# Performance work log

Hardware: AMD Instinct MI355X
Metric: run time of the kernel (lower is better)

Reference implementation:

```python
import jax, jax.numpy as jnp
import numpy as np

N_MOV, N_CREW, N_CAST = 200000, 100000, 100000
E = 600000
H, OUT = 128, 16


def _sage(x_src, x_dst, src, dst, Wl, Wr, b, n_dst):
    # PyG SAGEConv: lin_l(mean_{j in N(i)} x_src[j]) + lin_r(x_dst[i]); bias lives in lin_l
    msg = jax.ops.segment_sum(x_src[src], dst, num_segments=n_dst)
    cnt = jax.ops.segment_sum(jnp.ones(src.shape, x_src.dtype), dst, num_segments=n_dst)
    agg = msg / jnp.maximum(cnt, 1.0)[:, None]
    return agg @ Wl + b + x_dst @ Wr


def setup_inputs() -> dict:
    key = jax.random.key(0)
    kit = iter(jax.random.split(key, 64))
    def rn(shape, s=0.05):
        return jax.random.normal(next(kit), shape, jnp.float32) * s
    inp = {
        'x_movies': rn((N_MOV, 128), 1.0),
        'x_crew': rn((N_CREW, 64), 1.0),
        'x_cast': rn((N_CAST, 64), 1.0),
        'src_cm': jax.random.randint(next(kit), (E,), 0, N_CREW),
        'dst_cm': jax.random.randint(next(kit), (E,), 0, N_MOV),
        'src_am': jax.random.randint(next(kit), (E,), 0, N_CAST),
        'dst_am': jax.random.randint(next(kit), (E,), 0, N_MOV),
    }
    # (src_dim, dst_dim) per relation at layer 0; layer 1 uses H for both
    dims = {'cm': (64, 128), 'am': (64, 128), 'mc': (128, 64), 'ma': (128, 64)}
    for l in range(2):
        for rel, (ds, dd) in dims.items():
            if l > 0:
                ds, dd = H, H
            inp[f'Wl_{rel}_{l}'] = rn((ds, H))
            inp[f'Wr_{rel}_{l}'] = rn((dd, H))
            inp[f'b_{rel}_{l}'] = jnp.zeros((H,), jnp.float32)
    inp['lin_W'] = rn((H, OUT))
    inp['lin_b'] = jnp.zeros((OUT,), jnp.float32)
    return inp


def reference(x_movies, x_crew, x_cast, src_cm, dst_cm, src_am, dst_am,
              Wl_cm_0, Wr_cm_0, b_cm_0, Wl_am_0, Wr_am_0, b_am_0,
              Wl_mc_0, Wr_mc_0, b_mc_0, Wl_ma_0, Wr_ma_0, b_ma_0,
              Wl_cm_1, Wr_cm_1, b_cm_1, Wl_am_1, Wr_am_1, b_am_1,
              Wl_mc_1, Wr_mc_1, b_mc_1, Wl_ma_1, Wr_ma_1, b_ma_1,
              lin_W, lin_b):
    params = [
        {'cm': (Wl_cm_0, Wr_cm_0, b_cm_0), 'am': (Wl_am_0, Wr_am_0, b_am_0),
         'mc': (Wl_mc_0, Wr_mc_0, b_mc_0), 'ma': (Wl_ma_0, Wr_ma_0, b_ma_0)},
        {'cm': (Wl_cm_1, Wr_cm_1, b_cm_1), 'am': (Wl_am_1, Wr_am_1, b_am_1),
         'mc': (Wl_mc_1, Wr_mc_1, b_mc_1), 'ma': (Wl_ma_1, Wr_ma_1, b_ma_1)},
    ]
    xm, xc, xa = x_movies, x_crew, x_cast
    for p in params:  # dropout is identity in eval mode
        # movies receives from crew and cast; HeteroConv aggr='mean' over the 2 relations
        m = 0.5 * (_sage(xc, xm, src_cm, dst_cm, *p['cm'], N_MOV)
                   + _sage(xa, xm, src_am, dst_am, *p['am'], N_MOV))
        # reverse relations: movies -> crew / cast (flip edge direction)
        c = _sage(xm, xc, dst_cm, src_cm, *p['mc'], N_CREW)
        a = _sage(xm, xa, dst_am, src_am, *p['ma'], N_CAST)
        xm, xc, xa = jax.nn.relu(m), jax.nn.relu(c), jax.nn.relu(a)
    return xm @ lin_W + lin_b
```

## Files before the change

### kernel.cpp

```cpp
#include <hip/hip_runtime.h>

#define TPB 256
typedef unsigned int uint;
typedef unsigned short ushort;
typedef long long ll;
typedef __attribute__((ext_vector_type(8))) short bf16x8;
typedef __attribute__((ext_vector_type(8))) ushort u16x8;
typedef __attribute__((ext_vector_type(4))) float f32x4;

__device__ __forceinline__ float bf2f(ushort h) {
  return __uint_as_float(((uint)h) << 16);
}
__device__ __forceinline__ ushort f2bf(float f) {
  uint u = __float_as_uint(f);
  u += 0x7fffu + ((u >> 16) & 1u);
  return (ushort)(u >> 16);
}

__global__ __launch_bounds__(TPB) void convert_k(const float* __restrict__ x,
                                                 ushort* __restrict__ o, ll n8) {
  ll i = (ll)blockIdx.x * TPB + threadIdx.x;
  if (i >= n8) return;
  const float* p = x + i * 8;
  float4 a = *(const float4*)p;
  float4 b = *(const float4*)(p + 4);
  u16x8 v;
  v[0] = f2bf(a.x); v[1] = f2bf(a.y); v[2] = f2bf(a.z); v[3] = f2bf(a.w);
  v[4] = f2bf(b.x); v[5] = f2bf(b.y); v[6] = f2bf(b.z); v[7] = f2bf(b.w);
  *(u16x8*)&o[i * 8] = v;
}

__global__ __launch_bounds__(TPB) void rank_k(const int* __restrict__ src_cm,
                                              const int* __restrict__ dst_cm,
                                              const int* __restrict__ src_am,
                                              const int* __restrict__ dst_am, int E,
                                              int* __restrict__ cnt_m_cm,
                                              int* __restrict__ cnt_m_am,
                                              int* __restrict__ cnt_c,
                                              int* __restrict__ cnt_a,
                                              int* __restrict__ rk_m_cm,
                                              int* __restrict__ rk_c,
                                              int* __restrict__ rk_m_am,
                                              int* __restrict__ rk_a) {
  int i = blockIdx.x * blockDim.x + threadIdx.x;
  if (i < E) {
    rk_m_cm[i] = atomicAdd(&cnt_m_cm[dst_cm[i]], 1);
    rk_c[i]    = atomicAdd(&cnt_c[src_cm[i]], 1);
  } else if (i < 2 * E) {
    int e = i - E;
    rk_m_am[e] = atomicAdd(&cnt_m_am[dst_am[e]], 1);
    rk_a[e]    = atomicAdd(&cnt_a[src_am[e]], 1);
  }
}

__global__ __launch_bounds__(TPB) void rinvall_k(const int* __restrict__ cnt,
                                                 float* __restrict__ rinv,
                                                 int nm2, int total) {
  int i = blockIdx.x * blockDim.x + threadIdx.x;
  if (i < total) {
    float scale = (i < nm2) ? 0.5f : 1.0f;
    rinv[i] = scale / fmaxf((float)cnt[i], 1.0f);
  }
}

struct PJobs {
  const float* a[10];
  const float* bavg[10];
  ushort* out[10];
  const float* ba[2];
  const float* bb[2];
  float* bo[2];
};

__global__ __launch_bounds__(TPB) void prep_k(PJobs J) {
  int b = blockIdx.x;
  int t = threadIdx.x;
  if (b == 512) {
    if (t < 128) J.bo[0][t] = 0.5f * (J.ba[0][t] + J.bb[0][t]);
    else if (t < 256) J.bo[1][t - 128] = 0.5f * (J.ba[1][t - 128] + J.bb[1][t - 128]);
    return;
  }
  int job, idx, K;
  if (b < 384) { job = b >> 6; idx = ((b & 63) << 8) | t; K = 128; }
  else { int bb = b - 384; job = 6 + (bb >> 5); idx = ((bb & 31) << 8) | t; K = 64; }
  int col = idx / K, k = idx - col * K;
  float v = J.a[job][k * 128 + col];
  if (J.bavg[job]) v = 0.5f * (v + J.bavg[job][k * 128 + col]);
  J.out[job][idx] = f2bf(v);
}

__device__ __forceinline__ void rel_map(int b, int nb0, int nb1, int nb2, int nb3,
                                        int& r, int& lb) {
  if (b < nb0) { r = 0; lb = b; }
  else if (b < nb0 + nb1) { r = 1; lb = b - nb0; }
  else if (b < nb0 + nb1 + nb2) { r = 2; lb = b - nb0 - nb1; }
  else { r = 3; lb = b - nb0 - nb1 - nb2; }
}

__global__ __launch_bounds__(TPB) void blocksum_all_k(
    const int* __restrict__ c0, int n0, const int* __restrict__ c1, int n1,
    const int* __restrict__ c2, int n2, const int* __restrict__ c3, int n3,
    int* __restrict__ bsum) {
  __shared__ int lds[TPB];
  int nb0 = (n0 + TPB - 1) / TPB, nb1 = (n1 + TPB - 1) / TPB;
  int nb2 = (n2 + TPB - 1) / TPB, nb3 = (n3 + TPB - 1) / TPB;
  int r, lb;
  rel_map(blockIdx.x, nb0, nb1, nb2, nb3, r, lb);
  const int* cnt = (r == 0) ? c0 : (r == 1) ? c1 : (r == 2) ? c2 : c3;
  int n = (r == 0) ? n0 : (r == 1) ? n1 : (r == 2) ? n2 : n3;
  int t = threadIdx.x;
  int i = lb * TPB + t;
  lds[t] = (i < n) ? cnt[i] : 0;
  __syncthreads();
  for (int off = 128; off > 0; off >>= 1) {
    if (t < off) lds[t] += lds[t + off];
    __syncthreads();
  }
  if (t == 0) bsum[r * 1024 + lb] = lds[0];
}

__global__ __launch_bounds__(TPB) void scan_all_k(int* __restrict__ bsum,
                                                  int n0, int n1, int n2, int n3) {
  __shared__ int lds[TPB];
  int r = blockIdx.x;
  int n = (r == 0) ? n0 : (r == 1) ? n1 : (r == 2) ? n2 : n3;
  int nb = (n + TPB - 1) / TPB;
  int* bs = bsum + r * 1024;
  int t = threadIdx.x;
  int offset = 0;
  for (int base = 0; base < nb; base += TPB) {
    int v = (base + t < nb) ? bs[base + t] : 0;
    lds[t] = v;
    __syncthreads();
    for (int off = 1; off < TPB; off <<= 1) {
      int add = (t >= off) ? lds[t - off] : 0;
      __syncthreads();
      lds[t] += add;
      __syncthreads();
    }
    int incl = lds[t];
    if (base + t < nb) bs[base + t] = offset + incl - v;
    int tot = lds[TPB - 1];
    __syncthreads();
    offset += tot;
  }
}

__global__ __launch_bounds__(TPB) void finalize_all_k(
    const int* __restrict__ c0, int n0, int* __restrict__ rp0,
    const int* __restrict__ c1, int n1, int* __restrict__ rp1,
    const int* __restrict__ c2, int n2, int* __restrict__ rp2,
    const int* __restrict__ c3, int n3, int* __restrict__ rp3,
    const int* __restrict__ bsum) {
  __shared__ int lds[TPB];
  int nb0 = (n0 + TPB - 1) / TPB, nb1 = (n1 + TPB - 1) / TPB;
  int nb2 = (n2 + TPB - 1) / TPB, nb3 = (n3 + TPB - 1) / TPB;
  int r, lb;
  rel_map(blockIdx.x, nb0, nb1, nb2, nb3, r, lb);
  const int* cnt = (r == 0) ? c0 : (r == 1) ? c1 : (r == 2) ? c2 : c3;
  int* rowptr = (r == 0) ? rp0 : (r == 1) ? rp1 : (r == 2) ? rp2 : rp3;
  int n = (r == 0) ? n0 : (r == 1) ? n1 : (r == 2) ? n2 : n3;
  int t = threadIdx.x;
  int i = lb * TPB + t;
  int v = (i < n) ? cnt[i] : 0;
  lds[t] = v;
  __syncthreads();
  for (int off = 1; off < TPB; off <<= 1) {
    int add = (t >= off) ? lds[t - off] : 0;
    __syncthreads();
    lds[t] += add;
    __syncthreads();
  }
  int ex = lds[t] - v + bsum[r * 1024 + lb];
  if (i < n) {
    rowptr[i] = ex;
    if (i == n - 1) rowptr[n] = ex + v;
  }
}

__global__ __launch_bounds__(TPB) void fillr_k(const int* __restrict__ src_cm,
                                               const int* __restrict__ dst_cm,
                                               const int* __restrict__ src_am,
                                               const int* __restrict__ dst_am, int E,
                                               const int* __restrict__ rp_m_cm,
                                               const int* __restrict__ rp_m_am,
                                               const int* __restrict__ rp_c,
                                               const int* __restrict__ rp_a,
                                               const int* __restrict__ rk_m_cm,
                                               const int* __restrict__ rk_c,
                                               const int* __restrict__ rk_m_am,
                                               const int* __restrict__ rk_a,
                                               int* __restrict__ pm_m_cm,
                                               int* __restrict__ pm_m_am,
                                               int* __restrict__ pm_c,
                                               int* __restrict__ pm_a) {
  int i = blockIdx.x * blockDim.x + threadIdx.x;
  if (i < E) {
    int s = src_cm[i], d = dst_cm[i];
    pm_m_cm[rp_m_cm[d] + rk_m_cm[i]] = s;
    pm_c[rp_c[s] + rk_c[i]] = d;
  } else if (i < 2 * E) {
    int e = i - E;
    int s = src_am[e], d = dst_am[e];
    pm_m_am[rp_m_am[d] + rk_m_am[e]] = s;
    pm_a[rp_a[s] + rk_a[e]] = d;
  }
}

__global__ __launch_bounds__(TPB) void gatherw2_k(
    const ushort* __restrict__ xmh,
    const int* __restrict__ rp1, const int* __restrict__ pm1,
    const float* __restrict__ ri1, int N1, ushort* __restrict__ o1,
    const int* __restrict__ rp2, const int* __restrict__ pm2,
    const float* __restrict__ ri2, int N2, ushort* __restrict__ o2, int g1) {
  int b = blockIdx.x;
  const int* rowptr; const int* perm; const float* rinv; int N; ushort* out;
  int lb;
  if (b < g1) { rowptr = rp1; perm = pm1; rinv = ri1; N = N1; out = o1; lb = b; }
  else { rowptr = rp2; perm = pm2; rinv = ri2; N = N2; out = o2; lb = b - g1; }
  int nid = lb * 16 + (threadIdx.x >> 4);
  if (nid >= N) return;
  int d = (threadIdx.x & 15) << 3;
  int s0 = rowptr[nid], s1 = rowptr[nid + 1];
  float acc[8] = {0.f, 0.f, 0.f, 0.f, 0.f, 0.f, 0.f, 0.f};
  for (int j = s0; j < s1; ++j) {
    u16x8 v = *(const u16x8*)&xmh[((ll)perm[j] << 7) + d];
#pragma unroll
    for (int k = 0; k < 8; ++k) acc[k] += bf2f(v[k]);
  }
  float r = rinv[nid];
  u16x8 o;
#pragma unroll
  for (int k = 0; k < 8; ++k) o[k] = f2bf(acc[k] * r);
  *(u16x8*)&out[((ll)nid << 7) + d] = o;
}

__global__ __launch_bounds__(TPB) void gather2_k(
    const ushort* __restrict__ s1, const ushort* __restrict__ s2,
    const int* __restrict__ rp1, const int* __restrict__ pm1, const float* __restrict__ ri1,
    const int* __restrict__ rp2, const int* __restrict__ pm2, const float* __restrict__ ri2,
    int N, ushort* __restrict__ out) {
  int nid = blockIdx.x * 16 + (threadIdx.x >> 4);
  if (nid >= N) return;
  int d = (threadIdx.x & 15) << 3;
  float a1[8] = {0.f, 0.f, 0.f, 0.f, 0.f, 0.f, 0.f, 0.f};
  for (int j = rp1[nid]; j < rp1[nid + 1]; ++j) {
    u16x8 v = *(const u16x8*)&s1[((ll)pm1[j] << 7) + d];
#pragma unroll
    for (int k = 0; k < 8; ++k) a1[k] += bf2f(v[k]);
  }
  float a2[8] = {0.f, 0.f, 0.f, 0.f, 0.f, 0.f, 0.f, 0.f};
  for (int j = rp2[nid]; j < rp2[nid + 1]; ++j) {
    u16x8 v = *(const u16x8*)&s2[((ll)pm2[j] << 7) + d];
#pragma unroll
    for (int k = 0; k < 8; ++k) a2[k] += bf2f(v[k]);
  }
  float r1 = ri1[nid], r2 = ri2[nid];
  ushort* p = &out[((ll)nid << 7) + d];
  u16x8 cur = *(u16x8*)p;
  u16x8 o;
#pragma unroll
  for (int k = 0; k < 8; ++k) o[k] = f2bf(bf2f(cur[k]) + a1[k] * r1 + a2[k] * r2);
  *(u16x8*)p = o;
}

__global__ __launch_bounds__(TPB) void final_k(const ushort* __restrict__ X,
                                               const float* __restrict__ W,
                                               const float* __restrict__ b,
                                               float* __restrict__ out, int M) {
  __shared__ float lw[128 * 16];
  __shared__ float lb[16];
  int t = threadIdx.x;
  for (int i = t; i < 2048; i += TPB) lw[i] = W[i];
  if (t < 16) lb[t] = b[t];
  __syncthreads();
  ll row = (ll)blockIdx.x * TPB + t;
  if (row >= M) return;
  float acc[16];
#pragma unroll
  for (int c = 0; c < 16; ++c) acc[c] = lb[c];
  const ushort* xr = &X[row * 128];
  for (int k = 0; k < 128; k += 8) {
    u16x8 xv = *(const u16x8*)&xr[k];
#pragma unroll
    for (int j = 0; j < 8; ++j) {
      float xs = fmaxf(bf2f(xv[j]), 0.f);
#pragma unroll
      for (int c = 0; c < 16; ++c) acc[c] = fmaf(xs, lw[(k + j) * 16 + c], acc[c]);
    }
  }
#pragma unroll
  for (int c = 0; c < 16; c += 4) {
    float4 o; o.x = acc[c]; o.y = acc[c + 1]; o.z = acc[c + 2]; o.w = acc[c + 3];
    *(float4*)&out[row * 16 + c] = o;
  }
}

#define BK 64
#define XPITCH 72
#define CPITCH 132
struct CArgs {
  const void* X0; const ushort* WT0; int K0; int xb0;
  const void* X1; const ushort* WT1; int K1; int xb1;
  int nseg; const float* bias; void* out; int M; int nblk;
};

template <bool XRELU>
__global__ __launch_bounds__(TPB) void mfma3_k(CArgs a0, CArgs a1, CArgs a2) {
  const int bx = blockIdx.x;
  const CArgs& a = (bx < a0.nblk) ? a0 : (bx < a0.nblk + a1.nblk) ? a1 : a2;
  const int blk = (bx < a0.nblk) ? bx
                  : (bx < a0.nblk + a1.nblk) ? bx - a0.nblk
                                             : bx - a0.nblk - a1.nblk;

  __shared__ ushort sbuf[2 * 128 * XPITCH];
  ushort* Xs = sbuf;
  ushort* Ws = sbuf + 128 * XPITCH;
  const int t = threadIdx.x;
  const int lane = t & 63;
  const int wid = t >> 6;
  const int wm = (wid >> 1) << 6;
  const int wn = (wid & 1) << 6;
  const ll rbase = (ll)blk * 128;
  const int M = a.M;

  f32x4 acc[4][4];
#pragma unroll
  for (int mi = 0; mi < 4; ++mi)
#pragma unroll
    for (int ni = 0; ni < 4; ++ni) acc[mi][ni] = (f32x4){0.f, 0.f, 0.f, 0.f};

  for (int s = 0; s < a.nseg; ++s) {
    const void* Xv = s ? a.X1 : a.X0;
    const ushort* WT = s ? a.WT1 : a.WT0;
    const int K = s ? a.K1 : a.K0;
    const int xb = s ? a.xb1 : a.xb0;
    for (int k0 = 0; k0 < K; k0 += BK) {
      __syncthreads();
#pragma unroll
      for (int i = 0; i < 4; ++i) {
        int idx8 = t + i * TPB;
        int row = idx8 >> 3;
        int kb = (idx8 & 7) << 3;
        u16x8 xv;
        ll grow = rbase + row;
        if (grow < M) {
          if (xb) {
            xv = *(const u16x8*)((const ushort*)Xv + grow * K + k0 + kb);
            if (XRELU) {
#pragma unroll
              for (int j = 0; j < 8; ++j) xv[j] = (xv[j] & 0x8000u) ? (ushort)0 : xv[j];
            }
          } else {
            const float* xp = (const float*)Xv + grow * K + k0 + kb;
            float4 va = *(const float4*)xp;
            float4 vb = *(const float4*)(xp + 4);
            if (XRELU) {
              va.x = fmaxf(va.x, 0.f); va.y = fmaxf(va.y, 0.f);
              va.z = fmaxf(va.z, 0.f); va.w = fmaxf(va.w, 0.f);
              vb.x = fmaxf(vb.x, 0.f); vb.y = fmaxf(vb.y, 0.f);
              vb.z = fmaxf(vb.z, 0.f); vb.w = fmaxf(vb.w, 0.f);
            }
            xv[0] = f2bf(va.x); xv[1] = f2bf(va.y); xv[2] = f2bf(va.z); xv[3] = f2bf(va.w);
            xv[4] = f2bf(vb.x); xv[5] = f2bf(vb.y); xv[6] = f2bf(vb.z); xv[7] = f2bf(vb.w);
          }
        } else {
#pragma unroll
          for (int j = 0; j < 8; ++j) xv[j] = 0;
        }
        *(u16x8*)&Xs[row * XPITCH + kb] = xv;
        *(u16x8*)&Ws[row * XPITCH + kb] = *(const u16x8*)(WT + (ll)row * K + k0 + kb);
      }
      __syncthreads();
#pragma unroll
      for (int kk = 0; kk < BK; kk += 32) {
        const int krow = kk + ((lane >> 4) << 3);
        bf16x8 af[4], bfr[4];
#pragma unroll
        for (int mi = 0; mi < 4; ++mi)
          af[mi] = *(const bf16x8*)&Xs[(wm + mi * 16 + (lane & 15)) * XPITCH + krow];
#pragma unroll
        for (int ni = 0; ni < 4; ++ni)
          bfr[ni] = *(const bf16x8*)&Ws[(wn + ni * 16 + (lane & 15)) * XPITCH + krow];
#pragma unroll
        for (int mi = 0; mi < 4; ++mi)
#pragma unroll
          for (int ni = 0; ni < 4; ++ni)
            acc[mi][ni] = __builtin_amdgcn_mfma_f32_16x16x32_bf16(af[mi], bfr[ni],
                                                                  acc[mi][ni], 0, 0, 0);
      }
    }
  }

  __syncthreads();

  {
    const int colb = wn + (lane & 15);
    const int rsub = (lane >> 4) << 2;
#pragma unroll
    for (int ni = 0; ni < 4; ++ni) {
      int col = colb + ni * 16;
      float bv = a.bias ? a.bias[col] : 0.f;
#pragma unroll
      for (int mi = 0; mi < 4; ++mi) {
        int row0 = wm + mi * 16 + rsub;
#pragma unroll
        for (int j = 0; j < 4; ++j)
          sbuf[(row0 + j) * CPITCH + col] = f2bf(acc[mi][ni][j] + bv);
      }
    }
  }
  __syncthreads();
  {
    int lrow = t >> 1;
    int half = t & 1;
    ll grow = rbase + lrow;
    if (grow < M) {
      const ushort* src = &sbuf[lrow * CPITCH + half * 64];
      ushort* dst = (ushort*)a.out + grow * 128 + half * 64;
#pragma unroll
      for (int k = 0; k < 8; ++k)
        *(u16x8*)(dst + k * 8) = *(const u16x8*)(src + k * 8);
    }
  }
}

extern "C" void kernel_launch(void* const* d_in, const int* in_sizes, int n_in,
                              void* d_out, int out_size, void* d_ws, size_t ws_size,
                              hipStream_t stream) {
  const float* xm = (const float*)d_in[0];
  const float* xc = (const float*)d_in[1];
  const float* xa = (const float*)d_in[2];
  const int* src_cm = (const int*)d_in[3];
  const int* dst_cm = (const int*)d_in[4];
  const int* src_am = (const int*)d_in[5];
  const int* dst_am = (const int*)d_in[6];
  const float* Wl_cm_0 = (const float*)d_in[7];
  const float* Wr_cm_0 = (const float*)d_in[8];
  const float* b_cm_0  = (const float*)d_in[9];
  const float* Wl_am_0 = (const float*)d_in[10];
  const float* Wr_am_0 = (const float*)d_in[11];
  const float* b_am_0  = (const float*)d_in[12];
  const float* Wl_mc_0 = (const float*)d_in[13];
  const float* Wr_mc_0 = (const float*)d_in[14];
  const float* b_mc_0  = (const float*)d_in[15];
  const float* Wl_ma_0 = (const float*)d_in[16];
  const float* Wr_ma_0 = (const float*)d_in[17];
  const float* b_ma_0  = (const float*)d_in[18];
  const float* Wl_cm_1 = (const float*)d_in[19];
  const float* Wr_cm_1 = (const float*)d_in[20];
  const float* b_cm_1  = (const float*)d_in[21];
  const float* Wl_am_1 = (const float*)d_in[22];
  const float* Wr_am_1 = (const float*)d_in[23];
  const float* b_am_1  = (const float*)d_in[24];
  const float* lin_W   = (const float*)d_in[31];
  const float* lin_b   = (const float*)d_in[32];

  const int NM = in_sizes[0] / 128;
  const int NC = in_sizes[1] / 64;
  const int NA = in_sizes[2] / 64;
  const int E  = in_sizes[3];
  const int SMAX = (NC > NA) ? NC : NA;

  float* base = (float*)d_ws;
  size_t o = 0;
  ushort* A = (ushort*)(base + o); o += (size_t)NM * 64;
  ushort* xmh = (ushort*)(base + o); o += (size_t)NM * 64;
  float* S = base + o; o += (size_t)SMAX * 128;
  ushort* B = (ushort*)(base + o); o += (size_t)NC * 64;
  ushort* C = (ushort*)(base + o); o += (size_t)NA * 64;
  int* cnt_m_cm = (int*)(base + o); o += NM;
  int* cnt_m_am = (int*)(base + o); o += NM;
  int* cnt_c    = (int*)(base + o); o += NC;
  int* cnt_a    = (int*)(base + o); o += NA;
  float* rinv_m_cm = base + o; o += NM;
  float* rinv_m_am = base + o; o += NM;
  float* rinv_c    = base + o; o += NC;
  float* rinv_a    = base + o; o += NA;
  int* rp_m_cm = (int*)(base + o); o += NM + 1;
  int* rp_m_am = (int*)(base + o); o += NM + 1;
  int* rp_c    = (int*)(base + o); o += NC + 1;
  int* rp_a    = (int*)(base + o); o += NA + 1;
  int* pm_m_cm = (int*)(base + o); o += E;
  int* pm_m_am = (int*)(base + o); o += E;
  int* pm_c    = (int*)(base + o); o += E;
  int* pm_a    = (int*)(base + o); o += E;
  int* bsum    = (int*)(base + o); o += 4096;
  float* b0c  = base + o; o += 128;
  float* b1c  = base + o; o += 128;
  ushort* WT_r0   = (ushort*)(base + o); o += 8192;
  ushort* WT_r1   = (ushort*)(base + o); o += 8192;
  ushort* WT_mc0l = (ushort*)(base + o); o += 8192;
  ushort* WT_ma0l = (ushort*)(base + o); o += 8192;
  ushort* WT_cm1  = (ushort*)(base + o); o += 8192;
  ushort* WT_am1  = (ushort*)(base + o); o += 8192;
  ushort* WT_mc0r = (ushort*)(base + o); o += 4096;
  ushort* WT_ma0r = (ushort*)(base + o); o += 4096;
  ushort* WT_cm0  = (ushort*)(base + o); o += 4096;
  ushort* WT_am0  = (ushort*)(base + o); o += 4096;

  if (ws_size < o * sizeof(float)) return;

  int* rk_m_cm = (int*)S;
  int* rk_c    = rk_m_cm + E;
  int* rk_m_am = rk_m_cm + 2 * E;
  int* rk_a    = rk_m_cm + 3 * E;
  ushort* S1h = (ushort*)S;
  ushort* S2h = S1h + (size_t)SMAX * 128;

  float* outf = (float*)d_out;
  const int g2E = (2 * E + TPB - 1) / TPB;
  const int nbm = (NM + TPB - 1) / TPB;
  const int nbc = (NC + TPB - 1) / TPB;
  const int nba = (NA + TPB - 1) / TPB;
  const int nbtot = 2 * nbm + nbc + nba;
  const int nodes_total = 2 * NM + NC + NA;

  {
    ll n8 = (ll)NM * 16;
    convert_k<<<(int)((n8 + TPB - 1) / TPB), TPB, 0, stream>>>(xm, xmh, n8);
  }

  hipMemsetAsync(cnt_m_cm, 0, sizeof(int) * (size_t)nodes_total, stream);
  rank_k<<<g2E, TPB, 0, stream>>>(src_cm, dst_cm, src_am, dst_am, E,
                                  cnt_m_cm, cnt_m_am, cnt_c, cnt_a,
                                  rk_m_cm, rk_c, rk_m_am, rk_a);
  rinvall_k<<<(nodes_total + TPB - 1) / TPB, TPB, 0, stream>>>(cnt_m_cm, rinv_m_cm,
                                                               2 * NM, nodes_total);

  PJobs J;
  J.a[0] = Wr_cm_0; J.bavg[0] = Wr_am_0; J.out[0] = WT_r0;
  J.a[1] = Wr_cm_1; J.bavg[1] = Wr_am_1; J.out[1] = WT_r1;
  J.a[2] = Wl_mc_0; J.bavg[2] = nullptr; J.out[2] = WT_mc0l;
  J.a[3] = Wl_ma_0; J.bavg[3] = nullptr; J.out[3] = WT_ma0l;
  J.a[4] = Wl_cm_1; J.bavg[4] = nullptr; J.out[4] = WT_cm1;
  J.a[5] = Wl_am_1; J.bavg[5] = nullptr; J.out[5] = WT_am1;
  J.a[6] = Wr_mc_0; J.bavg[6] = nullptr; J.out[6] = WT_mc0r;
  J.a[7] = Wr_ma_0; J.bavg[7] = nullptr; J.out[7] = WT_ma0r;
  J.a[8] = Wl_cm_0; J.bavg[8] = nullptr; J.out[8] = WT_cm0;
  J.a[9] = Wl_am_0; J.bavg[9] = nullptr; J.out[9] = WT_am0;
  J.ba[0] = b_cm_0; J.bb[0] = b_am_0; J.bo[0] = b0c;
  J.ba[1] = b_cm_1; J.bb[1] = b_am_1; J.bo[1] = b1c;
  prep_k<<<513, TPB, 0, stream>>>(J);

  blocksum_all_k<<<nbtot, TPB, 0, stream>>>(cnt_m_cm, NM, cnt_m_am, NM,
                                            cnt_c, NC, cnt_a, NA, bsum);
  scan_all_k<<<4, TPB, 0, stream>>>(bsum, NM, NM, NC, NA);
  finalize_all_k<<<nbtot, TPB, 0, stream>>>(cnt_m_cm, NM, rp_m_cm, cnt_m_am, NM, rp_m_am,
                                            cnt_c, NC, rp_c, cnt_a, NA, rp_a, bsum);
  fillr_k<<<g2E, TPB, 0, stream>>>(src_cm, dst_cm, src_am, dst_am, E,
                                   rp_m_cm, rp_m_am, rp_c, rp_a,
                                   rk_m_cm, rk_c, rk_m_am, rk_a,
                                   pm_m_cm, pm_m_am, pm_c, pm_a);

  const int gM = (NM + 127) / 128;
  const int gC = (NC + 127) / 128;
  const int gA = (NA + 127) / 128;
  const int gnM = (NM + 15) / 16;
  const int gwc = (NC + 15) / 16;
  const int gwa = (NA + 15) / 16;
  CArgs Z = {};

  gatherw2_k<<<gwc + gwa, TPB, 0, stream>>>(xmh, rp_c, pm_c, rinv_c, NC, S1h,
                                            rp_a, pm_a, rinv_a, NA, S2h, gwc);
  {
    CArgs ac = {S1h, WT_mc0l, 128, 1, xc, WT_mc0r, 64, 0, 2, b_mc_0, B, NC, gC};
    CArgs aa = {S2h, WT_ma0l, 128, 1, xa, WT_ma0r, 64, 0, 2, b_ma_0, C, NA, gA};
    CArgs am = {xmh, WT_r0, 128, 1, nullptr, nullptr, 0, 0, 1, b0c, A, NM, gM};
    mfma3_k<false><<<gC + gA + gM, TPB, 0, stream>>>(ac, aa, am);
  }
  {
    CArgs ac = {xc, WT_cm0, 64, 0, nullptr, nullptr, 0, 0, 1, nullptr, S1h, NC, gC};
    CArgs aa = {xa, WT_am0, 64, 0, nullptr, nullptr, 0, 0, 1, nullptr, S2h, NA, gA};
    mfma3_k<false><<<gC + gA, TPB, 0, stream>>>(ac, aa, Z);
  }
  gather2_k<<<gnM, TPB, 0, stream>>>(S1h, S2h, rp_m_cm, pm_m_cm, rinv_m_cm,
                                     rp_m_am, pm_m_am, rinv_m_am, NM, A);

  {
    CArgs am = {A, WT_r1, 128, 1, nullptr, nullptr, 0, 0, 1, b1c, A, NM, gM};
    CArgs ac = {B, WT_cm1, 128, 1, nullptr, nullptr, 0, 0, 1, nullptr, S1h, NC, gC};
    CArgs aa = {C, WT_am1, 128, 1, nullptr, nullptr, 0, 0, 1, nullptr, S2h, NA, gA};
    mfma3_k<true><<<gM + gC + gA, TPB, 0, stream>>>(am, ac, aa);
  }
  gather2_k<<<gnM, TPB, 0, stream>>>(S1h, S2h, rp_m_cm, pm_m_cm, rinv_m_cm,
                                     rp_m_am, pm_m_am, rinv_m_am, NM, A);

  final_k<<<(NM + TPB - 1) / TPB, TPB, 0, stream>>>(A, lin_W, lin_b, outf, NM);
}
```

Before: 585.6 us.

## Merge prep kernels, fuse layer-0 GEMM launches, and dual-accumulate gathers

Combines the bf16 conversion, degree-ranking atomics and weight-prep blocks into one launch, and folds the reciprocal-count computation into the block-sum kernel, which removes several small launches. The two layer-0 GEMM launches become one five-job launch by writing the crew/cast transforms to new scratch buffers (S3h/S4h), so they no longer overwrite S1h/S2h. The gather kernels unroll by two with separate accumulators to raise memory-level parallelism. The extra scratch buffers add workspace, and heterogeneous blocks in one launch may compete for resources.

```diff
diff --git a/kernel.cpp b/kernel.cpp
--- a/kernel.cpp
+++ b/kernel.cpp
@@ -15,52 +15,6 @@
   uint u = __float_as_uint(f);
   u += 0x7fffu + ((u >> 16) & 1u);
   return (ushort)(u >> 16);
-}
-
-__global__ __launch_bounds__(TPB) void convert_k(const float* __restrict__ x,
-                                                 ushort* __restrict__ o, ll n8) {
-  ll i = (ll)blockIdx.x * TPB + threadIdx.x;
-  if (i >= n8) return;
-  const float* p = x + i * 8;
-  float4 a = *(const float4*)p;
-  float4 b = *(const float4*)(p + 4);
-  u16x8 v;
-  v[0] = f2bf(a.x); v[1] = f2bf(a.y); v[2] = f2bf(a.z); v[3] = f2bf(a.w);
-  v[4] = f2bf(b.x); v[5] = f2bf(b.y); v[6] = f2bf(b.z); v[7] = f2bf(b.w);
-  *(u16x8*)&o[i * 8] = v;
-}
-
-__global__ __launch_bounds__(TPB) void rank_k(const int* __restrict__ src_cm,
-                                              const int* __restrict__ dst_cm,
-                                              const int* __restrict__ src_am,
-                                              const int* __restrict__ dst_am, int E,
-                                              int* __restrict__ cnt_m_cm,
-                                              int* __restrict__ cnt_m_am,
-                                              int* __restrict__ cnt_c,
-                                              int* __restrict__ cnt_a,
-                                              int* __restrict__ rk_m_cm,
-                                              int* __restrict__ rk_c,
-                                              int* __restrict__ rk_m_am,
-                                              int* __restrict__ rk_a) {
-  int i = blockIdx.x * blockDim.x + threadIdx.x;
-  if (i < E) {
-    rk_m_cm[i] = atomicAdd(&cnt_m_cm[dst_cm[i]], 1);
-    rk_c[i]    = atomicAdd(&cnt_c[src_cm[i]], 1);
-  } else if (i < 2 * E) {
-    int e = i - E;
-    rk_m_am[e] = atomicAdd(&cnt_m_am[dst_am[e]], 1);
-    rk_a[e]    = atomicAdd(&cnt_a[src_am[e]], 1);
-  }
-}
-
-__global__ __launch_bounds__(TPB) void rinvall_k(const int* __restrict__ cnt,
-                                                 float* __restrict__ rinv,
-                                                 int nm2, int total) {
-  int i = blockIdx.x * blockDim.x + threadIdx.x;
-  if (i < total) {
-    float scale = (i < nm2) ? 0.5f : 1.0f;
-    rinv[i] = scale / fmaxf((float)cnt[i], 1.0f);
-  }
 }
 
 struct PJobs {
@@ -72,9 +26,43 @@
   float* bo[2];
 };
 
-__global__ __launch_bounds__(TPB) void prep_k(PJobs J) {
+__global__ __launch_bounds__(TPB) void mega1_k(
+    const float* __restrict__ xm, ushort* __restrict__ xmh, ll n8, int gConv,
+    const int* __restrict__ src_cm, const int* __restrict__ dst_cm,
+    const int* __restrict__ src_am, const int* __restrict__ dst_am, int E, int g2E,
+    int* __restrict__ cnt_m_cm, int* __restrict__ cnt_m_am,
+    int* __restrict__ cnt_c, int* __restrict__ cnt_a,
+    int* __restrict__ rk_m_cm, int* __restrict__ rk_c,
+    int* __restrict__ rk_m_am, int* __restrict__ rk_a,
+    PJobs J) {
   int b = blockIdx.x;
   int t = threadIdx.x;
+  if (b < gConv) {
+    ll i = (ll)b * TPB + t;
+    if (i >= n8) return;
+    const float* p = xm + i * 8;
+    float4 a = *(const float4*)p;
+    float4 bb = *(const float4*)(p + 4);
+    u16x8 v;
+    v[0] = f2bf(a.x); v[1] = f2bf(a.y); v[2] = f2bf(a.z); v[3] = f2bf(a.w);
+    v[4] = f2bf(bb.x); v[5] = f2bf(bb.y); v[6] = f2bf(bb.z); v[7] = f2bf(bb.w);
+    *(u16x8*)&xmh[i * 8] = v;
+    return;
+  }
+  b -= gConv;
+  if (b < g2E) {
+    int i = b * TPB + t;
+    if (i < E) {
+      rk_m_cm[i] = atomicAdd(&cnt_m_cm[dst_cm[i]], 1);
+      rk_c[i]    = atomicAdd(&cnt_c[src_cm[i]], 1);
+    } else if (i < 2 * E) {
+      int e = i - E;
+      rk_m_am[e] = atomicAdd(&cnt_m_am[dst_am[e]], 1);
+      rk_a[e]    = atomicAdd(&cnt_a[src_am[e]], 1);
+    }
+    return;
+  }
+  b -= g2E;
   if (b == 512) {
     if (t < 128) J.bo[0][t] = 0.5f * (J.ba[0][t] + J.bb[0][t]);
     else if (t < 256) J.bo[1][t - 128] = 0.5f * (J.ba[1][t - 128] + J.bb[1][t - 128]);
@@ -82,7 +70,7 @@
   }
   int job, idx, K;
   if (b < 384) { job = b >> 6; idx = ((b & 63) << 8) | t; K = 128; }
-  else { int bb = b - 384; job = 6 + (bb >> 5); idx = ((bb & 31) << 8) | t; K = 64; }
+  else { int bb2 = b - 384; job = 6 + (bb2 >> 5); idx = ((bb2 & 31) << 8) | t; K = 64; }
   int col = idx / K, k = idx - col * K;
   float v = J.a[job][k * 128 + col];
   if (J.bavg[job]) v = 0.5f * (v + J.bavg[job][k * 128 + col]);
@@ -97,18 +85,27 @@
   else { r = 3; lb = b - nb0 - nb1 - nb2; }
 }
 
-__global__ __launch_bounds__(TPB) void blocksum_all_k(
+__global__ __launch_bounds__(TPB) void bsum_rinv_k(
     const int* __restrict__ c0, int n0, const int* __restrict__ c1, int n1,
     const int* __restrict__ c2, int n2, const int* __restrict__ c3, int n3,
-    int* __restrict__ bsum) {
+    int* __restrict__ bsum, float* __restrict__ rinv, int nm2, int total, int nbtot) {
   __shared__ int lds[TPB];
+  int b = blockIdx.x;
+  int t = threadIdx.x;
+  if (b >= nbtot) {
+    int i = (b - nbtot) * TPB + t;
+    if (i < total) {
+      float scale = (i < nm2) ? 0.5f : 1.0f;
+      rinv[i] = scale / fmaxf((float)c0[i], 1.0f);
+    }
+    return;
+  }
   int nb0 = (n0 + TPB - 1) / TPB, nb1 = (n1 + TPB - 1) / TPB;
   int nb2 = (n2 + TPB - 1) / TPB, nb3 = (n3 + TPB - 1) / TPB;
   int r, lb;
-  rel_map(blockIdx.x, nb0, nb1, nb2, nb3, r, lb);
+  rel_map(b, nb0, nb1, nb2, nb3, r, lb);
   const int* cnt = (r == 0) ? c0 : (r == 1) ? c1 : (r == 2) ? c2 : c3;
   int n = (r == 0) ? n0 : (r == 1) ? n1 : (r == 2) ? n2 : n3;
-  int t = threadIdx.x;
   int i = lb * TPB + t;
   lds[t] = (i < n) ? cnt[i] : 0;
   __syncthreads();
@@ -221,17 +218,23 @@
   int nid = lb * 16 + (threadIdx.x >> 4);
   if (nid >= N) return;
   int d = (threadIdx.x & 15) << 3;
-  int s0 = rowptr[nid], s1 = rowptr[nid + 1];
-  float acc[8] = {0.f, 0.f, 0.f, 0.f, 0.f, 0.f, 0.f, 0.f};
-  for (int j = s0; j < s1; ++j) {
-    u16x8 v = *(const u16x8*)&xmh[((ll)perm[j] << 7) + d];
-#pragma unroll
-    for (int k = 0; k < 8; ++k) acc[k] += bf2f(v[k]);
+  int j = rowptr[nid], e = rowptr[nid + 1];
+  float aA[8] = {0.f}, aB[8] = {0.f};
+  for (; j + 1 < e; j += 2) {
+    u16x8 v0 = *(const u16x8*)&xmh[((ll)perm[j] << 7) + d];
+    u16x8 v1 = *(const u16x8*)&xmh[((ll)perm[j + 1] << 7) + d];
+#pragma unroll
+    for (int k = 0; k < 8; ++k) { aA[k] += bf2f(v0[k]); aB[k] += bf2f(v1[k]); }
+  }
+  if (j < e) {
+    u16x8 v0 = *(const u16x8*)&xmh[((ll)perm[j] << 7) + d];
+#pragma unroll
+    for (int k = 0; k < 8; ++k) aA[k] += bf2f(v0[k]);
   }
   float r = rinv[nid];
   u16x8 o;
 #pragma unroll
-  for (int k = 0; k < 8; ++k) o[k] = f2bf(acc[k] * r);
+  for (int k = 0; k < 8; ++k) o[k] = f2bf((aA[k] + aB[k]) * r);
   *(u16x8*)&out[((ll)nid << 7) + d] = o;
 }
 
@@ -243,24 +246,47 @@
   int nid = blockIdx.x * 16 + (threadIdx.x >> 4);
   if (nid >= N) return;
   int d = (threadIdx.x & 15) << 3;
-  float a1[8] = {0.f, 0.f, 0.f, 0.f, 0.f, 0.f, 0.f, 0.f};
-  for (int j = rp1[nid]; j < rp1[nid + 1]; ++j) {
-    u16x8 v = *(const u16x8*)&s1[((ll)pm1[j] << 7) + d];
-#pragma unroll
-    for (int k = 0; k < 8; ++k) a1[k] += bf2f(v[k]);
-  }
-  float a2[8] = {0.f, 0.f, 0.f, 0.f, 0.f, 0.f, 0.f, 0.f};
-  for (int j = rp2[nid]; j < rp2[nid + 1]; ++j) {
-    u16x8 v = *(const u16x8*)&s2[((ll)pm2[j] << 7) + d];
-#pragma unroll
-    for (int k = 0; k < 8; ++k) a2[k] += bf2f(v[k]);
-  }
-  float r1 = ri1[nid], r2 = ri2[nid];
+  float aA[8] = {0.f}, aB[8] = {0.f};
+  {
+    int j = rp1[nid], e = rp1[nid + 1];
+    for (; j + 1 < e; j += 2) {
+      u16x8 v0 = *(const u16x8*)&s1[((ll)pm1[j] << 7) + d];
+      u16x8 v1 = *(const u16x8*)&s1[((ll)pm1[j + 1] << 7) + d];
+#pragma unroll
+      for (int k = 0; k < 8; ++k) { aA[k] += bf2f(v0[k]); aB[k] += bf2f(v1[k]); }
+    }
+    if (j < e) {
+      u16x8 v0 = *(const u16x8*)&s1[((ll)pm1[j] << 7) + d];
+#pragma unroll
+      for (int k = 0; k < 8; ++k) aA[k] += bf2f(v0[k]);
+    }
+  }
+  float r1 = ri1[nid];
+  float res[8];
+#pragma unroll
+  for (int k = 0; k < 8; ++k) res[k] = (aA[k] + aB[k]) * r1;
+  float bA[8] = {0.f}, bB[8] = {0.f};
+  {
+    int j = rp2[nid], e = rp2[nid + 1];
+    for (; j + 1 < e; j += 2) {
+      u16x8 v0 = *(const u16x8*)&s2[((ll)pm2[j] << 7) + d];
+      u16x8 v1 = *(const u16x8*)&s2[((ll)pm2[j + 1] << 7) + d];
+#pragma unroll
+      for (int k = 0; k < 8; ++k) { bA[k] += bf2f(v0[k]); bB[k] += bf2f(v1[k]); }
+    }
+    if (j < e) {
+      u16x8 v0 = *(const u16x8*)&s2[((ll)pm2[j] << 7) + d];
+#pragma unroll
+      for (int k = 0; k < 8; ++k) bA[k] += bf2f(v0[k]);
+    }
+  }
+  float r2 = ri2[nid];
   ushort* p = &out[((ll)nid << 7) + d];
   u16x8 cur = *(u16x8*)p;
   u16x8 o;
 #pragma unroll
-  for (int k = 0; k < 8; ++k) o[k] = f2bf(bf2f(cur[k]) + a1[k] * r1 + a2[k] * r2);
+  for (int k = 0; k < 8; ++k)
+    o[k] = f2bf(bf2f(cur[k]) + res[k] + (bA[k] + bB[k]) * r2);
   *(u16x8*)p = o;
 }
 
@@ -306,12 +332,14 @@
 };
 
 template <bool XRELU>
-__global__ __launch_bounds__(TPB) void mfma3_k(CArgs a0, CArgs a1, CArgs a2) {
+__global__ __launch_bounds__(TPB) void mfma5_k(CArgs a0, CArgs a1, CArgs a2,
+                                               CArgs a3, CArgs a4) {
   const int bx = blockIdx.x;
-  const CArgs& a = (bx < a0.nblk) ? a0 : (bx < a0.nblk + a1.nblk) ? a1 : a2;
-  const int blk = (bx < a0.nblk) ? bx
-                  : (bx < a0.nblk + a1.nblk) ? bx - a0.nblk
-                                             : bx - a0.nblk - a1.nblk;
+  const int o0 = a0.nblk, o1 = o0 + a1.nblk, o2 = o1 + a2.nblk, o3 = o2 + a3.nblk;
+  const CArgs& a = (bx < o0) ? a0 : (bx < o1) ? a1 : (bx < o2) ? a2
+                   : (bx < o3) ? a3 : a4;
+  const int blk = bx - ((bx < o0) ? 0 : (bx < o1) ? o0 : (bx < o2) ? o1
+                        : (bx < o3) ? o2 : o3);
 
   __shared__ ushort sbuf[2 * 128 * XPITCH];
   ushort* Xs = sbuf;
@@ -467,6 +495,8 @@
   ushort* A = (ushort*)(base + o); o += (size_t)NM * 64;
   ushort* xmh = (ushort*)(base + o); o += (size_t)NM * 64;
   float* S = base + o; o += (size_t)SMAX * 128;
+  ushort* S3h = (ushort*)(base + o); o += (size_t)SMAX * 64;
+  ushort* S4h = (ushort*)(base + o); o += (size_t)SMAX * 64;
   ushort* B = (ushort*)(base + o); o += (size_t)NC * 64;
   ushort* C = (ushort*)(base + o); o += (size_t)NA * 64;
   int* cnt_m_cm = (int*)(base + o); o += NM;
@@ -515,18 +545,8 @@
   const int nba = (NA + TPB - 1) / TPB;
   const int nbtot = 2 * nbm + nbc + nba;
   const int nodes_total = 2 * NM + NC + NA;
-
-  {
-    ll n8 = (ll)NM * 16;
-    convert_k<<<(int)((n8 + TPB - 1) / TPB), TPB, 0, stream>>>(xm, xmh, n8);
-  }
-
-  hipMemsetAsync(cnt_m_cm, 0, sizeof(int) * (size_t)nodes_total, stream);
-  rank_k<<<g2E, TPB, 0, stream>>>(src_cm, dst_cm, src_am, dst_am, E,
-                                  cnt_m_cm, cnt_m_am, cnt_c, cnt_a,
-                                  rk_m_cm, rk_c, rk_m_am, rk_a);
-  rinvall_k<<<(nodes_total + TPB - 1) / TPB, TPB, 0, stream>>>(cnt_m_cm, rinv_m_cm,
-                                                               2 * NM, nodes_total);
+  const ll n8 = (ll)NM * 16;
+  const int gConv = (int)((n8 + TPB - 1) / TPB);
 
   PJobs J;
   J.a[0] = Wr_cm_0; J.bavg[0] = Wr_am_0; J.out[0] = WT_r0;
@@ -541,10 +561,18 @@
   J.a[9] = Wl_am_0; J.bavg[9] = nullptr; J.out[9] = WT_am0;
   J.ba[0] = b_cm_0; J.bb[0] = b_am_0; J.bo[0] = b0c;
   J.ba[1] = b_cm_1; J.bb[1] = b_am_1; J.bo[1] = b1c;
-  prep_k<<<513, TPB, 0, stream>>>(J);
-
-  blocksum_all_k<<<nbtot, TPB, 0, stream>>>(cnt_m_cm, NM, cnt_m_am, NM,
-                                            cnt_c, NC, cnt_a, NA, bsum);
+
+  hipMemsetAsync(cnt_m_cm, 0, sizeof(int) * (size_t)nodes_total, stream);
+  mega1_k<<<gConv + g2E + 513, TPB, 0, stream>>>(
+      xm, xmh, n8, gConv, src_cm, dst_cm, src_am, dst_am, E, g2E,
+      cnt_m_cm, cnt_m_am, cnt_c, cnt_a, rk_m_cm, rk_c, rk_m_am, rk_a, J);
+
+  {
+    int gR = (nodes_total + TPB - 1) / TPB;
+    bsum_rinv_k<<<nbtot + gR, TPB, 0, stream>>>(cnt_m_cm, NM, cnt_m_am, NM,
+                                                cnt_c, NC, cnt_a, NA, bsum,
+                                                rinv_m_cm, 2 * NM, nodes_total, nbtot);
+  }
   scan_all_k<<<4, TPB, 0, stream>>>(bsum, NM, NM, NC, NA);
   finalize_all_k<<<nbtot, TPB, 0, stream>>>(cnt_m_cm, NM, rp_m_cm, cnt_m_am, NM, rp_m_am,
                                             cnt_c, NC, rp_c, cnt_a, NA, rp_a, bsum);
@@ -567,23 +595,20 @@
     CArgs ac = {S1h, WT_mc0l, 128, 1, xc, WT_mc0r, 64, 0, 2, b_mc_0, B, NC, gC};
     CArgs aa = {S2h, WT_ma0l, 128, 1, xa, WT_ma0r, 64, 0, 2, b_ma_0, C, NA, gA};
     CArgs am = {xmh, WT_r0, 128, 1, nullptr, nullptr, 0, 0, 1, b0c, A, NM, gM};
-    mfma3_k<false><<<gC + gA + gM, TPB, 0, stream>>>(ac, aa, am);
-  }
-  {
-    CArgs ac = {xc, WT_cm0, 64, 0, nullptr, nullptr, 0, 0, 1, nullptr, S1h, NC, gC};
-    CArgs aa = {xa, WT_am0, 64, 0, nullptr, nullptr, 0, 0, 1, nullptr, S2h, NA, gA};
-    mfma3_k<false><<<gC + gA, TPB, 0, stream>>>(ac, aa, Z);
-  }
-  gather2_k<<<gnM, TPB, 0, stream>>>(S1h, S2h, rp_m_cm, pm_m_cm, rinv_m_cm,
+    CArgs tc = {xc, WT_cm0, 64, 0, nullptr, nullptr, 0, 0, 1, nullptr, S3h, NC, gC};
+    CArgs ta = {xa, WT_am0, 64, 0, nullptr, nullptr, 0, 0, 1, nullptr, S4h, NA, gA};
+    mfma5_k<false><<<gC + gA + gM + gC + gA, TPB, 0, stream>>>(ac, aa, am, tc, ta);
+  }
+  gather2_k<<<gnM, TPB, 0, stream>>>(S3h, S4h, rp_m_cm, pm_m_cm, rinv_m_cm,
                                      rp_m_am, pm_m_am, rinv_m_am, NM, A);
 
   {
     CArgs am = {A, WT_r1, 128, 1, nullptr, nullptr, 0, 0, 1, b1c, A, NM, gM};
-    CArgs ac = {B, WT_cm1, 128, 1, nullptr, nullptr, 0, 0, 1, nullptr, S1h, NC, gC};
-    CArgs aa = {C, WT_am1, 128, 1, nullptr, nullptr, 0, 0, 1, nullptr, S2h, NA, gA};
-    mfma3_k<true><<<gM + gC + gA, TPB, 0, stream>>>(am, ac, aa);
-  }
-  gather2_k<<<gnM, TPB, 0, stream>>>(S1h, S2h, rp_m_cm, pm_m_cm, rinv_m_cm,
+    CArgs ac = {B, WT_cm1, 128, 1, nullptr, nullptr, 0, 0, 1, nullptr, S3h, NC, gC};
+    CArgs aa = {C, WT_am1, 128, 1, nullptr, nullptr, 0, 0, 1, nullptr, S4h, NA, gA};
+    mfma5_k<true><<<gM + gC + gA, TPB, 0, stream>>>(am, ac, aa, Z, Z);
+  }
+  gather2_k<<<gnM, TPB, 0, stream>>>(S3h, S4h, rp_m_cm, pm_m_cm, rinv_m_cm,
                                      rp_m_am, pm_m_am, rinv_m_am, NM, A);
 
   final_k<<<(NM + TPB - 1) / TPB, TPB, 0, stream>>>(A, lin_W, lin_b, outf, NM);
```

After: 559.1 us. 4.5% less time.
